# Performance work log

Measured on AMD Instinct MI355X. Metric: run time of the kernel, lower is better.

## Reference

```python
import jax, jax.numpy as jnp
import numpy as np

D_MODEL = 1024
D_FF = 4096
N_EXPERTS = 8
TOP_K = 2

def setup_inputs() -> dict:
    key = jax.random.key(0)
    ks = jax.random.split(key, 8)
    s = 0.02
    return {
        "x": jax.random.normal(ks[0], (4, 2048, D_MODEL), dtype=jnp.float32),
        "W1": jax.random.normal(ks[1], (N_EXPERTS, D_MODEL, D_FF), dtype=jnp.float32) * s,
        "b1": jnp.zeros((N_EXPERTS, D_FF), dtype=jnp.float32),
        "W2": jax.random.normal(ks[2], (N_EXPERTS, D_FF, D_MODEL), dtype=jnp.float32) * s,
        "b2": jnp.zeros((N_EXPERTS, D_MODEL), dtype=jnp.float32),
        "Wg": jax.random.normal(ks[3], (D_MODEL, N_EXPERTS), dtype=jnp.float32) * s,
        "bg": jnp.zeros((N_EXPERTS,), dtype=jnp.float32),
    }

def reference(x, W1, b1, W2, b2, Wg, bg):
    B, S, D = x.shape
    # Gating network
    gate_logits = jnp.einsum('bsd,de->bse', x, Wg) + bg
    gate_probs = jax.nn.softmax(gate_logits, axis=-1)  # (B,S,E)
    # Top-k routing on softmax probs (matches torch.topk(F.softmax(logits)))
    top_k_probs, top_k_indices = jax.lax.top_k(gate_probs, TOP_K)  # (B,S,k)
    T = B * S
    x_flat = x.reshape(T, D)
    idx_flat = top_k_indices.reshape(T, TOP_K)
    prob_flat = top_k_probs.reshape(T, TOP_K)
    # Per-token combine weight for each expert: sum of top-k probs routed to it
    # combine[t, e] = sum_j prob_flat[t, j] * (idx_flat[t, j] == e)
    onehot = jax.nn.one_hot(idx_flat, N_EXPERTS, dtype=x.dtype)  # (T,k,E)
    combine = jnp.einsum('tk,tke->te', prob_flat, onehot)  # (T,E)
    out = jnp.zeros((T, D), dtype=x.dtype)
    for e in range(N_EXPERTS):  # static small loop over experts
        h = jax.nn.relu(x_flat @ W1[e] + b1[e])  # (T, d_ff)
        y = h @ W2[e] + b2[e]                    # (T, d_model)
        out = out + combine[:, e:e+1] * y
    return out.reshape(B, S, D), gate_probs
```

## Files before the change

kernel.cpp:

```cpp
#include <hip/hip_runtime.h>

#define D_MODEL 1024
#define D_FF    4096
#define N_EXP   8
#define BM 128
#define BN 128
#define BK 64

typedef __attribute__((ext_vector_type(8))) short bf16x8;
typedef __attribute__((ext_vector_type(4))) float f32x4;
typedef unsigned int u32;
typedef unsigned short ushortT;

__device__ __forceinline__ unsigned short f2bf(float f) {
  union { float f; unsigned u; } v; v.f = f;
  unsigned r = v.u + 0x7FFFu + ((v.u >> 16) & 1u);
  return (unsigned short)(r >> 16);
}

__device__ __forceinline__ void gl_lds16(const void* g, void* l) {
  __builtin_amdgcn_global_load_lds((const __attribute__((address_space(1))) u32*)g,
                                   (__attribute__((address_space(3))) u32*)l, 16, 0, 0);
}

__global__ void convert_x_kernel(const float* __restrict__ x,
                                 unsigned short* __restrict__ xb, int total8) {
  int i = blockIdx.x * blockDim.x + threadIdx.x;
  if (i >= total8) return;
  const float4* src = (const float4*)x + (size_t)i * 2;
  float4 a = src[0], b = src[1];
  ushort4 lo, hi;
  lo.x = f2bf(a.x); lo.y = f2bf(a.y); lo.z = f2bf(a.z); lo.w = f2bf(a.w);
  hi.x = f2bf(b.x); hi.y = f2bf(b.y); hi.z = f2bf(b.z); hi.w = f2bf(b.w);
  ushort4* dst = (ushort4*)xb + (size_t)i * 2;
  dst[0] = lo; dst[1] = hi;
}

__global__ __launch_bounds__(256)
void transpose_convert_kernel(const float* __restrict__ src, unsigned short* __restrict__ dst,
                              int Ksub, int Nsrc, int k0, int n0, int Nchunk,
                              unsigned long long eStride) {
  __shared__ unsigned short s[64][65];
  int e = blockIdx.z;
  int kb = blockIdx.x * 64, nb = blockIdx.y * 64;
  const float* se = src + (size_t)e * eStride;
  unsigned short* de = dst + (size_t)e * Nchunk * Ksub;
  int tid = threadIdx.x;
  int lk = tid >> 4, ln = (tid & 15) * 4;
  #pragma unroll
  for (int p = 0; p < 4; p++) {
    int k = lk + p * 16;
    float4 v = *(const float4*)(se + (size_t)(k0 + kb + k) * Nsrc + (n0 + nb + ln));
    s[ln + 0][k] = f2bf(v.x);
    s[ln + 1][k] = f2bf(v.y);
    s[ln + 2][k] = f2bf(v.z);
    s[ln + 3][k] = f2bf(v.w);
  }
  __syncthreads();
  #pragma unroll
  for (int c = 0; c < 2; c++) {
    int id = tid + c * 256;
    int n = id >> 3, kc = id & 7;
    unsigned short u[8];
    #pragma unroll
    for (int j = 0; j < 8; j++) u[j] = s[n][kc * 8 + j];
    *(uint4*)(de + (size_t)(nb + n) * Ksub + kb + kc * 8) = *(const uint4*)u;
  }
}

__global__ void gating_kernel(const float* __restrict__ x,
                              const float* __restrict__ Wg,
                              const float* __restrict__ bg,
                              float* __restrict__ gate_out,
                              int* __restrict__ cnt,
                              int* __restrict__ tokIdx,
                              float* __restrict__ tokW, int T) {
  int wv = threadIdx.x >> 6, lane = threadIdx.x & 63;
  int t = blockIdx.x * 4 + wv;
  if (t >= T) return;
  const float* xr = x + (size_t)t * D_MODEL + lane * 16;
  float acc[N_EXP];
  #pragma unroll
  for (int e = 0; e < N_EXP; e++) acc[e] = 0.f;
  #pragma unroll
  for (int q = 0; q < 4; q++) {
    float4 xv = *(const float4*)(xr + q * 4);
    #pragma unroll
    for (int r = 0; r < 4; r++) {
      float xs = ((const float*)&xv)[r];
      const float* wrow = Wg + (size_t)(lane * 16 + q * 4 + r) * N_EXP;
      float4 wa = *(const float4*)wrow;
      float4 wb = *(const float4*)(wrow + 4);
      acc[0] += xs * wa.x; acc[1] += xs * wa.y; acc[2] += xs * wa.z; acc[3] += xs * wa.w;
      acc[4] += xs * wb.x; acc[5] += xs * wb.y; acc[6] += xs * wb.z; acc[7] += xs * wb.w;
    }
  }
  #pragma unroll
  for (int off = 32; off > 0; off >>= 1) {
    #pragma unroll
    for (int e = 0; e < N_EXP; e++) acc[e] += __shfl_xor(acc[e], off);
  }
  if (lane == 0) {
    float l[N_EXP], p[N_EXP];
    float m = -1e30f;
    #pragma unroll
    for (int e = 0; e < N_EXP; e++) { l[e] = acc[e] + bg[e]; m = fmaxf(m, l[e]); }
    float s = 0.f;
    #pragma unroll
    for (int e = 0; e < N_EXP; e++) { p[e] = __expf(l[e] - m); s += p[e]; }
    float inv = 1.f / s;
    #pragma unroll
    for (int e = 0; e < N_EXP; e++) { p[e] *= inv; gate_out[(size_t)t * N_EXP + e] = p[e]; }
    int e1 = 0;
    #pragma unroll
    for (int e = 1; e < N_EXP; e++) if (p[e] > p[e1]) e1 = e;
    int e2 = (e1 == 0) ? 1 : 0;
    #pragma unroll
    for (int e = 0; e < N_EXP; e++) if (e != e1 && p[e] > p[e2]) e2 = e;
    int pos = atomicAdd(cnt + e1, 1);
    tokIdx[(size_t)e1 * T + pos] = t; tokW[(size_t)e1 * T + pos] = p[e1];
    pos = atomicAdd(cnt + e2, 1);
    tokIdx[(size_t)e2 * T + pos] = t; tokW[(size_t)e2 * T + pos] = p[e2];
  }
}

__global__ void schedule_kernel(const int* __restrict__ cnt, int* __restrict__ meta,
                                int* __restrict__ tE, int* __restrict__ tB,
                                int* __restrict__ tV, int T, int maxTiles) {
  if (threadIdx.x != 0 || blockIdx.x != 0) return;
  int t = 0;
  for (int e = 0; e < N_EXP; e++) {
    int c = cnt[e];
    for (int r = 0; r < c && t < maxTiles; r += BM) {
      tE[t] = e; tB[t] = e * T + r; tV[t] = min(BM, c - r); t++;
    }
  }
  meta[0] = t;
}

__global__ __launch_bounds__(256)
void gemm1_kernel(const unsigned short* __restrict__ xb,
                  const unsigned short* __restrict__ w1t,
                  const float* __restrict__ b1,
                  const int* __restrict__ meta,
                  const int* __restrict__ tE, const int* __restrict__ tB,
                  const int* __restrict__ tV, const int* __restrict__ tokIdx,
                  unsigned short* __restrict__ h, int FFC, int chunk_off, int ncolLog2) {
  __shared__ unsigned short As[BM * BK];
  __shared__ unsigned short Bs[BN * BK];
  __shared__ int stok[BM];

  int total = gridDim.x * gridDim.y;
  int L = blockIdx.y * gridDim.x + blockIdx.x;
  int q = total >> 3, r8 = total & 7;
  int xcd = L & 7, idx = L >> 3;
  int work = (xcd < r8) ? (xcd * (q + 1) + idx) : (r8 * (q + 1) + (xcd - r8) * q + idx);
  int ncol = 1 << ncolLog2;
  int tile = work >> ncolLog2;
  int cb = work & (ncol - 1);
  if (tile >= meta[0]) return;
  int e = tE[tile], base = tB[tile], valid = tV[tile];
  int tid = threadIdx.x;

  if (tid < BM) stok[tid] = tokIdx[base + (tid < valid ? tid : valid - 1)];
  __syncthreads();

  int w = tid >> 6, lane = tid & 63;
  int lr = lane >> 3, lc = lane & 7;

  const unsigned short* panel = w1t + (size_t)e * FFC * D_MODEL;
  const unsigned short* aBase[4];
  const unsigned short* bBase[4];
  #pragma unroll
  for (int p = 0; p < 4; p++) {
    int row = (w * 4 + p) * 8 + lr;
    int cA = (lc - row) & 7;
    aBase[p] = xb + (size_t)stok[row] * D_MODEL + cA * 8;
    int cB = (lc - row) & 7;
    bBase[p] = panel + (size_t)(cb * BN + row) * D_MODEL + cB * 8;
  }

  int wr = w >> 1, wc = w & 1;
  int l15 = lane & 15, l4 = lane >> 4;
  int aOff[2][4], bOff[2][4];
  #pragma unroll
  for (int kk = 0; kk < 2; kk++) {
    #pragma unroll
    for (int m = 0; m < 4; m++) {
      int row = wr * 64 + m * 16 + l15;
      int c = kk * 4 + l4;
      aOff[kk][m] = row * 64 + (((c + row) & 7) << 3);
      int col = wc * 64 + m * 16 + l15;
      bOff[kk][m] = col * 64 + (((c + col) & 7) << 3);
    }
  }

  f32x4 acc[4][4];
  #pragma unroll
  for (int m = 0; m < 4; m++)
    #pragma unroll
    for (int n = 0; n < 4; n++) acc[m][n] = (f32x4){0.f, 0.f, 0.f, 0.f};

  for (int kt = 0; kt < D_MODEL / BK; kt++) {
    #pragma unroll
    for (int p = 0; p < 4; p++)
      gl_lds16(aBase[p] + kt * BK, &As[(w * 4 + p) * 512]);
    #pragma unroll
    for (int p = 0; p < 4; p++)
      gl_lds16(bBase[p] + kt * BK, &Bs[(w * 4 + p) * 512]);
    __syncthreads();
    #pragma unroll
    for (int kk = 0; kk < 2; kk++) {
      bf16x8 a[4], b[4];
      #pragma unroll
      for (int m = 0; m < 4; m++) a[m] = *(const bf16x8*)&As[aOff[kk][m]];
      #pragma unroll
      for (int n = 0; n < 4; n++) b[n] = *(const bf16x8*)&Bs[bOff[kk][n]];
      #pragma unroll
      for (int m = 0; m < 4; m++)
        #pragma unroll
        for (int n = 0; n < 4; n++)
          acc[m][n] = __builtin_amdgcn_mfma_f32_16x16x32_bf16(a[m], b[n], acc[m][n], 0, 0, 0);
    }
    __syncthreads();
  }

  #pragma unroll
  for (int n = 0; n < 4; n++) {
    int colc = cb * BN + wc * 64 + n * 16 + l15;
    float bias = b1[(size_t)e * D_FF + chunk_off + colc];
    #pragma unroll
    for (int m = 0; m < 4; m++) {
      #pragma unroll
      for (int r = 0; r < 4; r++) {
        int row = wr * 64 + m * 16 + l4 * 4 + r;
        float v = acc[m][n][r] + bias;
        v = v > 0.f ? v : 0.f;
        h[(size_t)(tile * BM + row) * FFC + colc] = f2bf(v);
      }
    }
  }
}

__global__ __launch_bounds__(256)
void gemm2_kernel(const unsigned short* __restrict__ h,
                  const unsigned short* __restrict__ w2t,
                  const float* __restrict__ b2,
                  const int* __restrict__ meta,
                  const int* __restrict__ tE, const int* __restrict__ tB,
                  const int* __restrict__ tV, const int* __restrict__ tokIdx,
                  const float* __restrict__ tokW,
                  float* __restrict__ out, int FFC, int chunk_off) {
  __shared__ unsigned short As[BM * BK];
  __shared__ unsigned short Bs[BN * BK];
  __shared__ int stok[BM];
  __shared__ float sw[BM];

  int total = gridDim.x * gridDim.y;
  int L = blockIdx.y * gridDim.x + blockIdx.x;
  int q = total >> 3, r8 = total & 7;
  int xcd = L & 7, idx = L >> 3;
  int work = (xcd < r8) ? (xcd * (q + 1) + idx) : (r8 * (q + 1) + (xcd - r8) * q + idx);
  int tile = work >> 3;
  int cb = work & 7;
  if (tile >= meta[0]) return;
  int e = tE[tile], base = tB[tile], valid = tV[tile];
  int tid = threadIdx.x;

  if (tid < BM) {
    int rr = tid < valid ? tid : valid - 1;
    stok[tid] = tokIdx[base + rr];
    sw[tid] = tokW[base + rr];
  }
  __syncthreads();

  int w = tid >> 6, lane = tid & 63;
  int lr = lane >> 3, lc = lane & 7;

  const unsigned short* panel = w2t + (size_t)e * D_MODEL * FFC;
  const unsigned short* aBase[4];
  const unsigned short* bBase[4];
  #pragma unroll
  for (int p = 0; p < 4; p++) {
    int row = (w * 4 + p) * 8 + lr;
    int cA = (lc - row) & 7;
    aBase[p] = h + (size_t)(tile * BM + row) * FFC + cA * 8;
    int cB = (lc - row) & 7;
    bBase[p] = panel + (size_t)(cb * BN + row) * FFC + cB * 8;
  }

  int wr = w >> 1, wc = w & 1;
  int l15 = lane & 15, l4 = lane >> 4;
  int aOff[2][4], bOff[2][4];
  #pragma unroll
  for (int kk = 0; kk < 2; kk++) {
    #pragma unroll
    for (int m = 0; m < 4; m++) {
      int row = wr * 64 + m * 16 + l15;
      int c = kk * 4 + l4;
      aOff[kk][m] = row * 64 + (((c + row) & 7) << 3);
      int col = wc * 64 + m * 16 + l15;
      bOff[kk][m] = col * 64 + (((c + col) & 7) << 3);
    }
  }

  f32x4 acc[4][4];
  #pragma unroll
  for (int m = 0; m < 4; m++)
    #pragma unroll
    for (int n = 0; n < 4; n++) acc[m][n] = (f32x4){0.f, 0.f, 0.f, 0.f};

  int KT = FFC / BK;
  for (int kt = 0; kt < KT; kt++) {
    #pragma unroll
    for (int p = 0; p < 4; p++)
      gl_lds16(aBase[p] + kt * BK, &As[(w * 4 + p) * 512]);
    #pragma unroll
    for (int p = 0; p < 4; p++)
      gl_lds16(bBase[p] + kt * BK, &Bs[(w * 4 + p) * 512]);
    __syncthreads();
    #pragma unroll
    for (int kk = 0; kk < 2; kk++) {
      bf16x8 a[4], b[4];
      #pragma unroll
      for (int m = 0; m < 4; m++) a[m] = *(const bf16x8*)&As[aOff[kk][m]];
      #pragma unroll
      for (int n = 0; n < 4; n++) b[n] = *(const bf16x8*)&Bs[bOff[kk][n]];
      #pragma unroll
      for (int m = 0; m < 4; m++)
        #pragma unroll
        for (int n = 0; n < 4; n++)
          acc[m][n] = __builtin_amdgcn_mfma_f32_16x16x32_bf16(a[m], b[n], acc[m][n], 0, 0, 0);
    }
    __syncthreads();
  }

  int addBias = (chunk_off == 0) ? 1 : 0;
  #pragma unroll
  for (int n = 0; n < 4; n++) {
    int colg = cb * BN + wc * 64 + n * 16 + l15;
    float bias = addBias ? b2[(size_t)e * D_MODEL + colg] : 0.f;
    #pragma unroll
    for (int m = 0; m < 4; m++) {
      #pragma unroll
      for (int r = 0; r < 4; r++) {
        int row = wr * 64 + m * 16 + l4 * 4 + r;
        if (row < valid) {
          float v = (acc[m][n][r] + bias) * sw[row];
          atomicAdd(out + (size_t)stok[row] * D_MODEL + colg, v);
        }
      }
    }
  }
}

extern "C" void kernel_launch(void* const* d_in, const int* in_sizes, int n_in,
                              void* d_out, int out_size, void* d_ws, size_t ws_size,
                              hipStream_t stream) {
  const float* x  = (const float*)d_in[0];
  const float* W1 = (const float*)d_in[1];
  const float* b1 = (const float*)d_in[2];
  const float* W2 = (const float*)d_in[3];
  const float* b2 = (const float*)d_in[4];
  const float* Wg = (const float*)d_in[5];
  const float* bg = (const float*)d_in[6];

  int T = in_sizes[0] / D_MODEL;
  float* out = (float*)d_out;
  float* gate_out = out + (size_t)T * D_MODEL;

  char* ws = (char*)d_ws;
  int* cnt  = (int*)(ws + 0);
  int* meta = (int*)(ws + 64);
  int* tE   = (int*)(ws + 128);
  int* tB   = (int*)(ws + 1024);
  int* tV   = (int*)(ws + 2048);
  size_t off = 4096;
  int* tokIdx = (int*)(ws + off);   off += (size_t)N_EXP * T * 4;
  float* tokW = (float*)(ws + off); off += (size_t)N_EXP * T * 4;
  unsigned short* xb = (unsigned short*)(ws + off); off += (size_t)T * D_MODEL * 2;
  off = (off + 255) & ~(size_t)255;

  int maxTiles = (2 * T) / BM + N_EXP;
  int FFC = D_FF;
  while (FFC > 256 &&
         off + (size_t)FFC * (16384 + 16384 + (size_t)maxTiles * BM * 2) > ws_size)
    FFC >>= 1;

  unsigned short* w1t = (unsigned short*)(ws + off); off += (size_t)FFC * 16384;
  unsigned short* w2t = (unsigned short*)(ws + off); off += (size_t)FFC * 16384;
  unsigned short* h   = (unsigned short*)(ws + off);

  hipMemsetAsync(d_out, 0, (size_t)T * D_MODEL * sizeof(float), stream);
  hipMemsetAsync(cnt, 0, N_EXP * sizeof(int), stream);

  int total8 = T * D_MODEL / 8;
  convert_x_kernel<<<(total8 + 255) / 256, 256, 0, stream>>>(x, xb, total8);
  gating_kernel<<<(T + 3) / 4, 256, 0, stream>>>(x, Wg, bg, gate_out, cnt, tokIdx, tokW, T);
  schedule_kernel<<<1, 64, 0, stream>>>(cnt, meta, tE, tB, tV, T, maxTiles);

  int ncol1Log2 = __builtin_ctz(FFC / BN);
  for (int c = 0; c * FFC < D_FF; c++) {
    transpose_convert_kernel<<<dim3(D_MODEL / 64, FFC / 64, N_EXP), 256, 0, stream>>>(
        W1, w1t, D_MODEL, D_FF, 0, c * FFC, FFC, (unsigned long long)D_MODEL * D_FF);
    transpose_convert_kernel<<<dim3(FFC / 64, D_MODEL / 64, N_EXP), 256, 0, stream>>>(
        W2, w2t, FFC, D_MODEL, c * FFC, 0, D_MODEL, (unsigned long long)D_FF * D_MODEL);
    gemm1_kernel<<<dim3(maxTiles, FFC / BN), 256, 0, stream>>>(
        xb, w1t, b1, meta, tE, tB, tV, tokIdx, h, FFC, c * FFC, ncol1Log2);
    gemm2_kernel<<<dim3(maxTiles, D_MODEL / BN), 256, 0, stream>>>(
        h, w2t, b2, meta, tE, tB, tV, tokIdx, tokW, out, FFC, c * FFC);
  }
}
```

Baseline: 794.6 us.

## Use 256x256 tiles with 8-wave ping-pong pipelined MFMA loop and split-K gemm2

Both expert GEMMs move to 256x256 tiles with 512 threads and double-buffered LDS (128KB). An eight-phase schedule interleaves global-to-LDS staging, LDS reads and MFMA bursts, with barriers and setprio so that loads overlap compute. gemm2 also splits K in two, keeping the grid large enough now that tiles are bigger. Because BM changes, maxTiles shrinks, so more padded rows are wasted on experts with small token counts. The schedule and the 128KB LDS footprint add risk and can limit occupancy.

```diff
diff --git a/kernel.cpp b/kernel.cpp
--- a/kernel.cpp
+++ b/kernel.cpp
@@ -3,14 +3,13 @@
 #define D_MODEL 1024
 #define D_FF    4096
 #define N_EXP   8
-#define BM 128
-#define BN 128
+#define BM 256
+#define BN 256
 #define BK 64
 
 typedef __attribute__((ext_vector_type(8))) short bf16x8;
 typedef __attribute__((ext_vector_type(4))) float f32x4;
 typedef unsigned int u32;
-typedef unsigned short ushortT;
 
 __device__ __forceinline__ unsigned short f2bf(float f) {
   union { float f; unsigned u; } v; v.f = f;
@@ -138,20 +137,83 @@
   meta[0] = t;
 }
 
-__global__ __launch_bounds__(256)
+#define RD_A(buf, qm) { _Pragma("unroll") for (int m_ = 0; m_ < 4; m_++) { \
+    int row_ = (qm)*128 + wm64 + m_*16 + l15; \
+    _Pragma("unroll") for (int kk_ = 0; kk_ < 2; kk_++) \
+      a[m_][kk_] = *(const bf16x8*)&AB[(buf)*16384 + row_*64 + (((kk_*4 + l4 + row_)&7)<<3)]; } }
+
+#define RD_B(buf, qn) { _Pragma("unroll") for (int n_ = 0; n_ < 2; n_++) { \
+    int rb_ = (qn)*128 + wn32 + n_*16 + l15; \
+    _Pragma("unroll") for (int kk_ = 0; kk_ < 2; kk_++) \
+      b[n_][kk_] = *(const bf16x8*)&BB[(buf)*16384 + rb_*64 + (((kk_*4 + l4 + rb_)&7)<<3)]; } }
+
+#define MQ(qm, qn) { _Pragma("unroll") for (int m_ = 0; m_ < 4; m_++) \
+    _Pragma("unroll") for (int n_ = 0; n_ < 2; n_++) { \
+      acc[qm][qn][m_][n_] = __builtin_amdgcn_mfma_f32_16x16x32_bf16(a[m_][0], b[n_][0], acc[qm][qn][m_][n_], 0, 0, 0); \
+      acc[qm][qn][m_][n_] = __builtin_amdgcn_mfma_f32_16x16x32_bf16(a[m_][1], b[n_][1], acc[qm][qn][m_][n_], 0, 0, 0); } }
+
+#define STG_A(buf, h, kt) do { \
+    gl_lds16(srcA[h][0] + (kt)*BK, &AB[(buf)*16384 + ((h)*128 + w*16 + 0)*64]); \
+    gl_lds16(srcA[h][1] + (kt)*BK, &AB[(buf)*16384 + ((h)*128 + w*16 + 8)*64]); } while (0)
+
+#define STG_B(buf, h, kt) do { \
+    gl_lds16(srcB[h][0] + (kt)*BK, &BB[(buf)*16384 + ((h)*128 + w*16 + 0)*64]); \
+    gl_lds16(srcB[h][1] + (kt)*BK, &BB[(buf)*16384 + ((h)*128 + w*16 + 8)*64]); } while (0)
+
+#define BAR_MID() { __builtin_amdgcn_s_barrier(); \
+    asm volatile("s_waitcnt lgkmcnt(0)" ::: "memory"); \
+    __builtin_amdgcn_sched_barrier(0); __builtin_amdgcn_s_setprio(1); }
+#define BAR_END() { __builtin_amdgcn_s_setprio(0); \
+    __builtin_amdgcn_s_barrier(); asm volatile("" ::: "memory"); }
+#define BAR_END_VM() { __builtin_amdgcn_s_setprio(0); \
+    asm volatile("s_waitcnt vmcnt(4)" ::: "memory"); \
+    __builtin_amdgcn_sched_barrier(0); \
+    __builtin_amdgcn_s_barrier(); asm volatile("" ::: "memory"); }
+
+#define EIGHT_PHASES(NT, NI) \
+  for (int i_ = 0; i_ < (NI); ++i_) { \
+    int kt0 = 2 * i_; \
+    int kb1 = kt0 + 1; \
+    int kb2 = (kt0 + 2 < (NT)) ? kt0 + 2 : 0; \
+    int kb3 = (kt0 + 3 < (NT)) ? kt0 + 3 : 0; \
+    RD_A(0, 0); RD_B(0, 0); STG_A(1, 0, kb1); STG_B(1, 1, kb1); \
+    BAR_MID(); MQ(0, 0); BAR_END(); \
+    RD_A(0, 1); \
+    BAR_MID(); MQ(1, 0); BAR_END(); \
+    RD_B(0, 1); STG_B(0, 0, kb2); \
+    BAR_MID(); MQ(1, 1); BAR_END(); \
+    RD_A(0, 0); STG_A(0, 1, kb2); \
+    BAR_MID(); MQ(0, 1); BAR_END_VM(); \
+    RD_A(1, 0); RD_B(1, 0); STG_A(0, 0, kb2); STG_B(0, 1, kb2); \
+    BAR_MID(); MQ(0, 0); BAR_END(); \
+    RD_A(1, 1); \
+    BAR_MID(); MQ(1, 0); BAR_END(); \
+    RD_B(1, 1); STG_B(1, 0, kb3); \
+    BAR_MID(); MQ(1, 1); BAR_END(); \
+    RD_A(1, 0); STG_A(1, 1, kb3); \
+    BAR_MID(); MQ(0, 1); BAR_END_VM(); \
+  }
+
+#define PROLOGUE_STAGES() do { \
+    STG_B(0, 0, 0); STG_A(0, 1, 0); STG_A(0, 0, 0); STG_B(0, 1, 0); \
+    STG_B(1, 0, 1); STG_A(1, 1, 1); \
+    asm volatile("s_waitcnt vmcnt(4)" ::: "memory"); \
+    __builtin_amdgcn_sched_barrier(0); \
+    __builtin_amdgcn_s_barrier(); asm volatile("" ::: "memory"); } while (0)
+
+__global__ __launch_bounds__(512, 2)
 void gemm1_kernel(const unsigned short* __restrict__ xb,
                   const unsigned short* __restrict__ w1t,
                   const float* __restrict__ b1,
                   const int* __restrict__ meta,
                   const int* __restrict__ tE, const int* __restrict__ tB,
                   const int* __restrict__ tV, const int* __restrict__ tokIdx,
-                  unsigned short* __restrict__ h, int FFC, int chunk_off, int ncolLog2) {
-  __shared__ unsigned short As[BM * BK];
-  __shared__ unsigned short Bs[BN * BK];
+                  unsigned short* __restrict__ hbuf, int FFC, int chunk_off, int ncolLog2) {
+  __shared__ unsigned short As[65536];
   __shared__ int stok[BM];
 
-  int total = gridDim.x * gridDim.y;
-  int L = blockIdx.y * gridDim.x + blockIdx.x;
+  int total = gridDim.x;
+  int L = blockIdx.x;
   int q = total >> 3, r8 = total & 7;
   int xcd = L & 7, idx = L >> 3;
   int work = (xcd < r8) ? (xcd * (q + 1) + idx) : (r8 * (q + 1) + (xcd - r8) * q + idx);
@@ -165,104 +227,85 @@
   if (tid < BM) stok[tid] = tokIdx[base + (tid < valid ? tid : valid - 1)];
   __syncthreads();
 
+  unsigned short* AB = As;
+  unsigned short* BB = As + 32768;
   int w = tid >> 6, lane = tid & 63;
-  int lr = lane >> 3, lc = lane & 7;
+  int wm = w >> 2, wn = w & 3;
+  int wm64 = wm * 64, wn32 = wn * 32;
+  int l15 = lane & 15, l4 = lane >> 4;
+  int sr = lane >> 3, scg = lane & 7;
 
   const unsigned short* panel = w1t + (size_t)e * FFC * D_MODEL;
-  const unsigned short* aBase[4];
-  const unsigned short* bBase[4];
-  #pragma unroll
-  for (int p = 0; p < 4; p++) {
-    int row = (w * 4 + p) * 8 + lr;
-    int cA = (lc - row) & 7;
-    aBase[p] = xb + (size_t)stok[row] * D_MODEL + cA * 8;
-    int cB = (lc - row) & 7;
-    bBase[p] = panel + (size_t)(cb * BN + row) * D_MODEL + cB * 8;
-  }
-
-  int wr = w >> 1, wc = w & 1;
-  int l15 = lane & 15, l4 = lane >> 4;
-  int aOff[2][4], bOff[2][4];
-  #pragma unroll
-  for (int kk = 0; kk < 2; kk++) {
-    #pragma unroll
-    for (int m = 0; m < 4; m++) {
-      int row = wr * 64 + m * 16 + l15;
-      int c = kk * 4 + l4;
-      aOff[kk][m] = row * 64 + (((c + row) & 7) << 3);
-      int col = wc * 64 + m * 16 + l15;
-      bOff[kk][m] = col * 64 + (((c + col) & 7) << 3);
-    }
-  }
-
-  f32x4 acc[4][4];
-  #pragma unroll
-  for (int m = 0; m < 4; m++)
-    #pragma unroll
-    for (int n = 0; n < 4; n++) acc[m][n] = (f32x4){0.f, 0.f, 0.f, 0.f};
-
-  for (int kt = 0; kt < D_MODEL / BK; kt++) {
-    #pragma unroll
-    for (int p = 0; p < 4; p++)
-      gl_lds16(aBase[p] + kt * BK, &As[(w * 4 + p) * 512]);
-    #pragma unroll
-    for (int p = 0; p < 4; p++)
-      gl_lds16(bBase[p] + kt * BK, &Bs[(w * 4 + p) * 512]);
-    __syncthreads();
-    #pragma unroll
-    for (int kk = 0; kk < 2; kk++) {
-      bf16x8 a[4], b[4];
-      #pragma unroll
-      for (int m = 0; m < 4; m++) a[m] = *(const bf16x8*)&As[aOff[kk][m]];
-      #pragma unroll
-      for (int n = 0; n < 4; n++) b[n] = *(const bf16x8*)&Bs[bOff[kk][n]];
+  const unsigned short* srcA[2][2];
+  const unsigned short* srcB[2][2];
+  #pragma unroll
+  for (int h = 0; h < 2; h++)
+    #pragma unroll
+    for (int j = 0; j < 2; j++) {
+      int r = h * 128 + w * 16 + j * 8 + sr;
+      int swz = ((scg - r) & 7) << 3;
+      srcA[h][j] = xb + (size_t)stok[r] * D_MODEL + swz;
+      srcB[h][j] = panel + (size_t)(cb * BN + r) * D_MODEL + swz;
+    }
+
+  f32x4 acc[2][2][4][2];
+  #pragma unroll
+  for (int qm = 0; qm < 2; qm++)
+    #pragma unroll
+    for (int qn = 0; qn < 2; qn++)
       #pragma unroll
       for (int m = 0; m < 4; m++)
         #pragma unroll
-        for (int n = 0; n < 4; n++)
-          acc[m][n] = __builtin_amdgcn_mfma_f32_16x16x32_bf16(a[m], b[n], acc[m][n], 0, 0, 0);
-    }
-    __syncthreads();
-  }
-
-  #pragma unroll
-  for (int n = 0; n < 4; n++) {
-    int colc = cb * BN + wc * 64 + n * 16 + l15;
-    float bias = b1[(size_t)e * D_FF + chunk_off + colc];
-    #pragma unroll
-    for (int m = 0; m < 4; m++) {
+        for (int n = 0; n < 2; n++) acc[qm][qn][m][n] = (f32x4){0.f, 0.f, 0.f, 0.f};
+
+  bf16x8 a[4][2], b[2][2];
+  const int nt = D_MODEL / BK;
+
+  PROLOGUE_STAGES();
+  EIGHT_PHASES(nt, nt / 2);
+
+  const float* b1e = b1 + (size_t)e * D_FF + chunk_off + cb * BN;
+  #pragma unroll
+  for (int qn = 0; qn < 2; qn++)
+    #pragma unroll
+    for (int n = 0; n < 2; n++) {
+      int colL = qn * 128 + wn32 + n * 16 + l15;
+      float bias = b1e[colL];
       #pragma unroll
-      for (int r = 0; r < 4; r++) {
-        int row = wr * 64 + m * 16 + l4 * 4 + r;
-        float v = acc[m][n][r] + bias;
-        v = v > 0.f ? v : 0.f;
-        h[(size_t)(tile * BM + row) * FFC + colc] = f2bf(v);
-      }
-    }
-  }
-}
-
-__global__ __launch_bounds__(256)
-void gemm2_kernel(const unsigned short* __restrict__ h,
+      for (int qm = 0; qm < 2; qm++)
+        #pragma unroll
+        for (int m = 0; m < 4; m++)
+          #pragma unroll
+          for (int r = 0; r < 4; r++) {
+            int row = qm * 128 + wm64 + m * 16 + l4 * 4 + r;
+            float v = acc[qm][qn][m][n][r] + bias;
+            v = v > 0.f ? v : 0.f;
+            hbuf[(size_t)(tile * BM + row) * FFC + cb * BN + colL] = f2bf(v);
+          }
+    }
+}
+
+__global__ __launch_bounds__(512, 2)
+void gemm2_kernel(const unsigned short* __restrict__ hbuf,
                   const unsigned short* __restrict__ w2t,
                   const float* __restrict__ b2,
                   const int* __restrict__ meta,
                   const int* __restrict__ tE, const int* __restrict__ tB,
                   const int* __restrict__ tV, const int* __restrict__ tokIdx,
                   const float* __restrict__ tokW,
-                  float* __restrict__ out, int FFC, int chunk_off) {
-  __shared__ unsigned short As[BM * BK];
-  __shared__ unsigned short Bs[BN * BK];
+                  float* __restrict__ out, int FFC, int chunk) {
+  __shared__ unsigned short As[65536];
   __shared__ int stok[BM];
   __shared__ float sw[BM];
 
-  int total = gridDim.x * gridDim.y;
-  int L = blockIdx.y * gridDim.x + blockIdx.x;
+  int total = gridDim.x;
+  int L = blockIdx.x;
   int q = total >> 3, r8 = total & 7;
   int xcd = L & 7, idx = L >> 3;
   int work = (xcd < r8) ? (xcd * (q + 1) + idx) : (r8 * (q + 1) + (xcd - r8) * q + idx);
   int tile = work >> 3;
-  int cb = work & 7;
+  int cb = (work >> 1) & 3;
+  int ks = work & 1;
   if (tile >= meta[0]) return;
   int e = tE[tile], base = tB[tile], valid = tV[tile];
   int tid = threadIdx.x;
@@ -274,84 +317,65 @@
   }
   __syncthreads();
 
+  unsigned short* AB = As;
+  unsigned short* BB = As + 32768;
   int w = tid >> 6, lane = tid & 63;
-  int lr = lane >> 3, lc = lane & 7;
+  int wm = w >> 2, wn = w & 3;
+  int wm64 = wm * 64, wn32 = wn * 32;
+  int l15 = lane & 15, l4 = lane >> 4;
+  int sr = lane >> 3, scg = lane & 7;
+
+  const int nt = FFC / BK / 2;
+  const int ksOff = ks * nt * BK;
 
   const unsigned short* panel = w2t + (size_t)e * D_MODEL * FFC;
-  const unsigned short* aBase[4];
-  const unsigned short* bBase[4];
-  #pragma unroll
-  for (int p = 0; p < 4; p++) {
-    int row = (w * 4 + p) * 8 + lr;
-    int cA = (lc - row) & 7;
-    aBase[p] = h + (size_t)(tile * BM + row) * FFC + cA * 8;
-    int cB = (lc - row) & 7;
-    bBase[p] = panel + (size_t)(cb * BN + row) * FFC + cB * 8;
-  }
-
-  int wr = w >> 1, wc = w & 1;
-  int l15 = lane & 15, l4 = lane >> 4;
-  int aOff[2][4], bOff[2][4];
-  #pragma unroll
-  for (int kk = 0; kk < 2; kk++) {
-    #pragma unroll
-    for (int m = 0; m < 4; m++) {
-      int row = wr * 64 + m * 16 + l15;
-      int c = kk * 4 + l4;
-      aOff[kk][m] = row * 64 + (((c + row) & 7) << 3);
-      int col = wc * 64 + m * 16 + l15;
-      bOff[kk][m] = col * 64 + (((c + col) & 7) << 3);
-    }
-  }
-
-  f32x4 acc[4][4];
-  #pragma unroll
-  for (int m = 0; m < 4; m++)
-    #pragma unroll
-    for (int n = 0; n < 4; n++) acc[m][n] = (f32x4){0.f, 0.f, 0.f, 0.f};
-
-  int KT = FFC / BK;
-  for (int kt = 0; kt < KT; kt++) {
-    #pragma unroll
-    for (int p = 0; p < 4; p++)
-      gl_lds16(aBase[p] + kt * BK, &As[(w * 4 + p) * 512]);
-    #pragma unroll
-    for (int p = 0; p < 4; p++)
-      gl_lds16(bBase[p] + kt * BK, &Bs[(w * 4 + p) * 512]);
-    __syncthreads();
-    #pragma unroll
-    for (int kk = 0; kk < 2; kk++) {
-      bf16x8 a[4], b[4];
-      #pragma unroll
-      for (int m = 0; m < 4; m++) a[m] = *(const bf16x8*)&As[aOff[kk][m]];
-      #pragma unroll
-      for (int n = 0; n < 4; n++) b[n] = *(const bf16x8*)&Bs[bOff[kk][n]];
+  const unsigned short* srcA[2][2];
+  const unsigned short* srcB[2][2];
+  #pragma unroll
+  for (int h = 0; h < 2; h++)
+    #pragma unroll
+    for (int j = 0; j < 2; j++) {
+      int r = h * 128 + w * 16 + j * 8 + sr;
+      int swz = ((scg - r) & 7) << 3;
+      srcA[h][j] = hbuf + (size_t)(tile * BM + r) * FFC + ksOff + swz;
+      srcB[h][j] = panel + (size_t)(cb * BN + r) * FFC + ksOff + swz;
+    }
+
+  f32x4 acc[2][2][4][2];
+  #pragma unroll
+  for (int qm = 0; qm < 2; qm++)
+    #pragma unroll
+    for (int qn = 0; qn < 2; qn++)
       #pragma unroll
       for (int m = 0; m < 4; m++)
         #pragma unroll
-        for (int n = 0; n < 4; n++)
-          acc[m][n] = __builtin_amdgcn_mfma_f32_16x16x32_bf16(a[m], b[n], acc[m][n], 0, 0, 0);
-    }
-    __syncthreads();
-  }
-
-  int addBias = (chunk_off == 0) ? 1 : 0;
-  #pragma unroll
-  for (int n = 0; n < 4; n++) {
-    int colg = cb * BN + wc * 64 + n * 16 + l15;
-    float bias = addBias ? b2[(size_t)e * D_MODEL + colg] : 0.f;
-    #pragma unroll
-    for (int m = 0; m < 4; m++) {
+        for (int n = 0; n < 2; n++) acc[qm][qn][m][n] = (f32x4){0.f, 0.f, 0.f, 0.f};
+
+  bf16x8 a[4][2], b[2][2];
+
+  PROLOGUE_STAGES();
+  EIGHT_PHASES(nt, nt / 2);
+
+  int addBias = (chunk == 0 && ks == 0) ? 1 : 0;
+  #pragma unroll
+  for (int qn = 0; qn < 2; qn++)
+    #pragma unroll
+    for (int n = 0; n < 2; n++) {
+      int colg = cb * BN + qn * 128 + wn32 + n * 16 + l15;
+      float bias = addBias ? b2[(size_t)e * D_MODEL + colg] : 0.f;
       #pragma unroll
-      for (int r = 0; r < 4; r++) {
-        int row = wr * 64 + m * 16 + l4 * 4 + r;
-        if (row < valid) {
-          float v = (acc[m][n][r] + bias) * sw[row];
-          atomicAdd(out + (size_t)stok[row] * D_MODEL + colg, v);
-        }
-      }
-    }
-  }
+      for (int qm = 0; qm < 2; qm++)
+        #pragma unroll
+        for (int m = 0; m < 4; m++)
+          #pragma unroll
+          for (int r = 0; r < 4; r++) {
+            int row = qm * 128 + wm64 + m * 16 + l4 * 4 + r;
+            if (row < valid) {
+              float v = (acc[qm][qn][m][n][r] + bias) * sw[row];
+              atomicAdd(out + (size_t)stok[row] * D_MODEL + colg, v);
+            }
+          }
+    }
 }
 
 extern "C" void kernel_launch(void* const* d_in, const int* in_sizes, int n_in,
@@ -399,15 +423,16 @@
   gating_kernel<<<(T + 3) / 4, 256, 0, stream>>>(x, Wg, bg, gate_out, cnt, tokIdx, tokW, T);
   schedule_kernel<<<1, 64, 0, stream>>>(cnt, meta, tE, tB, tV, T, maxTiles);
 
-  int ncol1Log2 = __builtin_ctz(FFC / BN);
+  int ncol1 = FFC / BN;
+  int ncol1Log2 = __builtin_ctz(ncol1);
   for (int c = 0; c * FFC < D_FF; c++) {
     transpose_convert_kernel<<<dim3(D_MODEL / 64, FFC / 64, N_EXP), 256, 0, stream>>>(
         W1, w1t, D_MODEL, D_FF, 0, c * FFC, FFC, (unsigned long long)D_MODEL * D_FF);
     transpose_convert_kernel<<<dim3(FFC / 64, D_MODEL / 64, N_EXP), 256, 0, stream>>>(
         W2, w2t, FFC, D_MODEL, c * FFC, 0, D_MODEL, (unsigned long long)D_FF * D_MODEL);
-    gemm1_kernel<<<dim3(maxTiles, FFC / BN), 256, 0, stream>>>(
+    gemm1_kernel<<<maxTiles * ncol1, 512, 0, stream>>>(
         xb, w1t, b1, meta, tE, tB, tV, tokIdx, h, FFC, c * FFC, ncol1Log2);
-    gemm2_kernel<<<dim3(maxTiles, D_MODEL / BN), 256, 0, stream>>>(
-        h, w2t, b2, meta, tE, tB, tV, tokIdx, tokW, out, FFC, c * FFC);
-  }
-}
+    gemm2_kernel<<<maxTiles * (D_MODEL / BN) * 2, 512, 0, stream>>>(
+        h, w2t, b2, meta, tE, tB, tV, tokIdx, tokW, out, FFC, c);
+  }
+}
```

Result: slower. 880.7 us (+10.8%).
